# Performance work log

Hardware: AMD Instinct MI355X
Metric: run time of the kernel (lower is better)

## Reference

```python
import jax, jax.numpy as jnp
import numpy as np

S, B, H2, M = 4096, 16, 1024, 4096  # seq_len, batch, 2*hidden_size, max_number_of_entries


def setup_inputs() -> dict:
    key = jax.random.key(0)
    ks = jax.random.split(key, 5)
    return {
        "encoder_outputs": jax.random.normal(ks[0], (S, B, H2), jnp.float32),
        "state": jax.random.normal(ks[1], (B, H2), jnp.float32),
        "previous_attention": jax.random.uniform(ks[2], (B, M), jnp.float32),
        "attn_w": jax.random.normal(ks[3], (H2, H2), jnp.float32) / np.sqrt(H2).astype(np.float32),
        "attn_b": jnp.zeros((H2,), jnp.float32),
        "time_w": jax.random.normal(ks[4], (M, M), jnp.float32) / np.sqrt(M).astype(np.float32),
        "time_b": jnp.zeros((M,), jnp.float32),
    }


def reference(encoder_outputs, state, previous_attention, attn_w, attn_b, time_w, time_b):
    # encoder_outputs: [S, B, 2H]; state: [B, 2H]; previous_attention: [B, M]
    seq_len = encoder_outputs.shape[0]
    # attend(): Linear on state, then per-timestep dot product with encoder output.
    # The original Python loop over S timesteps + torch.cat is one batched matvec:
    altered_state = state @ attn_w.T + attn_b                      # [B, 2H]
    weights = jnp.einsum('bd,sbd->bs', altered_state, encoder_outputs)  # [B, S]
    # time_attention branch (its result is computed but unused by the outputs,
    # mirrored here for faithfulness to the original forward)
    apw = previous_attention @ time_w.T + time_b                   # [B, M]
    prev_probs = jax.nn.softmax(apw[:, :seq_len], axis=0)          # softmax over batch dim, as in original
    _adjusted_weights = prev_probs * weights                       # dead value in the original module
    # final softmax attention + weighted sum over encoder outputs
    normalized_weights = jax.nn.softmax(weights, axis=1)           # [B, S]
    attention_applied = jnp.einsum('bs,sbd->bd', normalized_weights, encoder_outputs)  # [B, 2H]
    return attention_applied, normalized_weights
```

## Files before the change

kernel.cpp:

```cpp
#include <hip/hip_runtime.h>
#include <cstdint>
#include <cstddef>

#define S_LEN 4096
#define B_SZ 16
#define H2D 1024
#define P_PER_B 256

__device__ __forceinline__ float dot4(float4 a, float4 b) {
    return a.x * b.x + a.y * b.y + a.z * b.z + a.w * b.w;
}
__device__ __forceinline__ void axpy4(float4& acc, float w, float4 v) {
    acc.x += w * v.x; acc.y += w * v.y; acc.z += w * v.z; acc.w += w * v.w;
}

__global__ __launch_bounds__(256) void k_altered(const float* __restrict__ state,
                                                 const float* __restrict__ attn_w,
                                                 const float* __restrict__ attn_b,
                                                 float* __restrict__ altered) {
    const int i = (blockIdx.x * 256 + threadIdx.x) >> 6;
    const int lane = threadIdx.x & 63;
    const float4* w4 = (const float4*)(attn_w + (size_t)i * H2D);
    float4 r[4];
#pragma unroll
    for (int j = 0; j < 4; ++j) r[j] = w4[lane + 64 * j];
    const float bias = attn_b[i];
    for (int b = 0; b < B_SZ; ++b) {
        const float4* s4 = (const float4*)(state + b * H2D);
        float p = 0.f;
#pragma unroll
        for (int j = 0; j < 4; ++j) p += dot4(r[j], s4[lane + 64 * j]);
#pragma unroll
        for (int off = 32; off; off >>= 1) p += __shfl_xor(p, off, 64);
        if (lane == 0) altered[b * H2D + i] = p + bias;
    }
}

__global__ __launch_bounds__(256) void k_pass1(const float* __restrict__ enc,
                                               const float* __restrict__ altered,
                                               float* __restrict__ w_raw) {
    const int b = blockIdx.y;
    const int wave = threadIdx.x >> 6, lane = threadIdx.x & 63;
    const int slot = blockIdx.x * 4 + wave;
    const float4* a4p = (const float4*)(altered + b * H2D);
    float4 af[4];
#pragma unroll
    for (int j = 0; j < 4; ++j) af[j] = a4p[lane + 64 * j];
    const int s0 = slot * 16;
    for (int k = 0; k < 16; k += 4) {
        float4 e[4][4];
#pragma unroll
        for (int r = 0; r < 4; ++r) {
            const float4* e4 = (const float4*)(enc + ((size_t)(s0 + k + r) * B_SZ + b) * H2D);
#pragma unroll
            for (int j = 0; j < 4; ++j) e[r][j] = e4[lane + 64 * j];
        }
        float p[4];
#pragma unroll
        for (int r = 0; r < 4; ++r) {
            p[r] = 0.f;
#pragma unroll
            for (int j = 0; j < 4; ++j) p[r] += dot4(af[j], e[r][j]);
        }
#pragma unroll
        for (int off = 32; off; off >>= 1) {
#pragma unroll
            for (int r = 0; r < 4; ++r) p[r] += __shfl_xor(p[r], off, 64);
        }
        if (lane == 0) {
#pragma unroll
            for (int r = 0; r < 4; ++r) w_raw[b * S_LEN + s0 + k + r] = p[r];
        }
    }
}

__global__ __launch_bounds__(1024) void k_softmax(const float* __restrict__ w_raw,
                                                  float* __restrict__ out_nw) {
    const int b = blockIdx.x, t = threadIdx.x;
    const int wave = t >> 6, lane = t & 63;
    __shared__ float sm[16], ss[16], sbc[2];
    float4 v = ((const float4*)(w_raw + b * S_LEN))[t];
    float m = fmaxf(fmaxf(v.x, v.y), fmaxf(v.z, v.w));
#pragma unroll
    for (int off = 32; off; off >>= 1) m = fmaxf(m, __shfl_xor(m, off, 64));
    if (lane == 0) sm[wave] = m;
    __syncthreads();
    if (t == 0) {
        float M = sm[0];
#pragma unroll
        for (int i = 1; i < 16; ++i) M = fmaxf(M, sm[i]);
        sbc[0] = M;
    }
    __syncthreads();
    const float M = sbc[0];
    float4 e;
    e.x = __expf(v.x - M); e.y = __expf(v.y - M);
    e.z = __expf(v.z - M); e.w = __expf(v.w - M);
    float s = e.x + e.y + e.z + e.w;
#pragma unroll
    for (int off = 32; off; off >>= 1) s += __shfl_xor(s, off, 64);
    if (lane == 0) ss[wave] = s;
    __syncthreads();
    if (t == 0) {
        float Z = 0.f;
#pragma unroll
        for (int i = 0; i < 16; ++i) Z += ss[i];
        sbc[1] = 1.f / Z;
    }
    __syncthreads();
    const float iZ = sbc[1];
    ((float4*)(out_nw + b * S_LEN))[t] = make_float4(e.x * iZ, e.y * iZ, e.z * iZ, e.w * iZ);
}

__global__ __launch_bounds__(256) void k_pass2(const float* __restrict__ enc,
                                               const float* __restrict__ nw,
                                               float* __restrict__ pacc) {
    const int b = blockIdx.y;
    const int wave = threadIdx.x >> 6, lane = threadIdx.x & 63;
    const int slot = blockIdx.x * 4 + wave;
    float4 acc[4];
#pragma unroll
    for (int j = 0; j < 4; ++j) acc[j] = make_float4(0.f, 0.f, 0.f, 0.f);
    const int s0 = slot * 16;
    for (int k = 0; k < 16; k += 4) {
        float4 e[4][4];
        float w[4];
#pragma unroll
        for (int r = 0; r < 4; ++r) {
            const int s = s0 + k + r;
            const float4* e4 = (const float4*)(enc + ((size_t)s * B_SZ + b) * H2D);
#pragma unroll
            for (int j = 0; j < 4; ++j) e[r][j] = e4[lane + 64 * j];
            w[r] = nw[b * S_LEN + s];
        }
#pragma unroll
        for (int r = 0; r < 4; ++r)
#pragma unroll
            for (int j = 0; j < 4; ++j) axpy4(acc[j], w[r], e[r][j]);
    }
    float4* o = (float4*)(pacc + (size_t)(b * P_PER_B + slot) * H2D);
#pragma unroll
    for (int j = 0; j < 4; ++j) o[lane + 64 * j] = acc[j];
}

__global__ __launch_bounds__(256) void k_comb1(const float* __restrict__ pacc,
                                               float* __restrict__ pacc2) {
    const int b = blockIdx.x >> 4, pg = blockIdx.x & 15, t = threadIdx.x;
    float4 s = make_float4(0.f, 0.f, 0.f, 0.f);
#pragma unroll
    for (int i = 0; i < 16; ++i) {
        const float4 v = ((const float4*)(pacc + (size_t)(b * P_PER_B + pg * 16 + i) * H2D))[t];
        s.x += v.x; s.y += v.y; s.z += v.z; s.w += v.w;
    }
    ((float4*)(pacc2 + (size_t)(b * 16 + pg) * H2D))[t] = s;
}

__global__ __launch_bounds__(64) void k_comb2(const float* __restrict__ pacc2,
                                              float* __restrict__ out_attn) {
    const int b = blockIdx.x >> 2;
    const int col = (blockIdx.x & 3) * 64 + threadIdx.x;
    float4 s = make_float4(0.f, 0.f, 0.f, 0.f);
#pragma unroll
    for (int i = 0; i < 16; ++i) {
        const float4 v = ((const float4*)(pacc2 + (size_t)(b * 16 + i) * H2D))[col];
        s.x += v.x; s.y += v.y; s.z += v.z; s.w += v.w;
    }
    ((float4*)(out_attn + b * H2D))[col] = s;
}

extern "C" void kernel_launch(void* const* d_in, const int* in_sizes, int n_in,
                              void* d_out, int out_size, void* d_ws, size_t ws_size,
                              hipStream_t stream) {
    const float* enc    = (const float*)d_in[0];
    const float* state  = (const float*)d_in[1];
    const float* attn_w = (const float*)d_in[3];
    const float* attn_b = (const float*)d_in[4];

    float* ws = (float*)d_ws;
    float* altered = ws;
    float* w_raw   = ws + 16384;
    float* pacc    = ws + 16384 + 65536;
    float* pacc2   = pacc + (size_t)B_SZ * P_PER_B * H2D;

    float* out_attn = (float*)d_out;
    float* out_nw   = (float*)d_out + B_SZ * H2D;

    hipLaunchKernelGGL(k_altered, dim3(256), dim3(256), 0, stream,
                       state, attn_w, attn_b, altered);
    hipLaunchKernelGGL(k_pass1, dim3(64, B_SZ), dim3(256), 0, stream,
                       enc, altered, w_raw);
    hipLaunchKernelGGL(k_softmax, dim3(B_SZ), dim3(1024), 0, stream,
                       w_raw, out_nw);
    hipLaunchKernelGGL(k_pass2, dim3(64, B_SZ), dim3(256), 0, stream,
                       enc, out_nw, pacc);
    hipLaunchKernelGGL(k_comb1, dim3(256), dim3(256), 0, stream,
                       pacc, pacc2);
    hipLaunchKernelGGL(k_comb2, dim3(64), dim3(64), 0, stream,
                       pacc2, out_attn);
}
```

Before: 450.0 us.

## Fuse score and weighted-sum passes with online softmax split-K combine

Merges the score pass and the weighted-sum pass into one flash-style kernel that keeps per-wave running max, sum and accumulator, so encoder outputs are streamed from memory once instead of twice. Finalization now rescales the per-slot partials by their exp-max correction, normalizes the weights, and reduces the partial accumulators with atomic adds. The exchange is extra exp/rescale arithmetic per chunk and a floating-point summation order that varies from run to run because of the atomics.

New measurement: 415.8 us. 7.6% less time.

```diff
diff --git a/kernel.cpp b/kernel.cpp
--- a/kernel.cpp
+++ b/kernel.cpp
@@ -36,26 +36,36 @@
     }
 }
 
-__global__ __launch_bounds__(256) void k_pass1(const float* __restrict__ enc,
+__global__ __launch_bounds__(256) void k_flash(const float* __restrict__ enc,
                                                const float* __restrict__ altered,
-                                               float* __restrict__ w_raw) {
+                                               float* __restrict__ w_raw,
+                                               float* __restrict__ pm,
+                                               float* __restrict__ pl,
+                                               float* __restrict__ pacc) {
     const int b = blockIdx.y;
     const int wave = threadIdx.x >> 6, lane = threadIdx.x & 63;
     const int slot = blockIdx.x * 4 + wave;
-    const float4* a4p = (const float4*)(altered + b * H2D);
+
+    const float4* a4 = (const float4*)(altered + b * H2D);
     float4 af[4];
 #pragma unroll
-    for (int j = 0; j < 4; ++j) af[j] = a4p[lane + 64 * j];
+    for (int j = 0; j < 4; ++j) af[j] = a4[lane + 64 * j];
+
+    float m = -1e30f, l = 0.f;
+    float4 acc[4];
+#pragma unroll
+    for (int j = 0; j < 4; ++j) acc[j] = make_float4(0.f, 0.f, 0.f, 0.f);
+
     const int s0 = slot * 16;
     for (int k = 0; k < 16; k += 4) {
         float4 e[4][4];
+        float p[4];
 #pragma unroll
         for (int r = 0; r < 4; ++r) {
             const float4* e4 = (const float4*)(enc + ((size_t)(s0 + k + r) * B_SZ + b) * H2D);
 #pragma unroll
             for (int j = 0; j < 4; ++j) e[r][j] = e4[lane + 64 * j];
         }
-        float p[4];
 #pragma unroll
         for (int r = 0; r < 4; ++r) {
             p[r] = 0.f;
@@ -63,109 +73,95 @@
             for (int j = 0; j < 4; ++j) p[r] += dot4(af[j], e[r][j]);
         }
 #pragma unroll
-        for (int off = 32; off; off >>= 1) {
+        for (int off = 32; off; off >>= 1)
 #pragma unroll
             for (int r = 0; r < 4; ++r) p[r] += __shfl_xor(p[r], off, 64);
-        }
         if (lane == 0) {
 #pragma unroll
             for (int r = 0; r < 4; ++r) w_raw[b * S_LEN + s0 + k + r] = p[r];
         }
+        float mn = m;
+#pragma unroll
+        for (int r = 0; r < 4; ++r) mn = fmaxf(mn, p[r]);
+        const float sc = __expf(m - mn);
+        float ex[4];
+#pragma unroll
+        for (int r = 0; r < 4; ++r) ex[r] = __expf(p[r] - mn);
+        l = l * sc + ex[0] + ex[1] + ex[2] + ex[3];
+#pragma unroll
+        for (int j = 0; j < 4; ++j) {
+            acc[j].x *= sc; acc[j].y *= sc; acc[j].z *= sc; acc[j].w *= sc;
+#pragma unroll
+            for (int r = 0; r < 4; ++r) axpy4(acc[j], ex[r], e[r][j]);
+        }
+        m = mn;
     }
-}
 
-__global__ __launch_bounds__(1024) void k_softmax(const float* __restrict__ w_raw,
-                                                  float* __restrict__ out_nw) {
-    const int b = blockIdx.x, t = threadIdx.x;
-    const int wave = t >> 6, lane = t & 63;
-    __shared__ float sm[16], ss[16], sbc[2];
-    float4 v = ((const float4*)(w_raw + b * S_LEN))[t];
-    float m = fmaxf(fmaxf(v.x, v.y), fmaxf(v.z, v.w));
-#pragma unroll
-    for (int off = 32; off; off >>= 1) m = fmaxf(m, __shfl_xor(m, off, 64));
-    if (lane == 0) sm[wave] = m;
-    __syncthreads();
-    if (t == 0) {
-        float M = sm[0];
-#pragma unroll
-        for (int i = 1; i < 16; ++i) M = fmaxf(M, sm[i]);
-        sbc[0] = M;
-    }
-    __syncthreads();
-    const float M = sbc[0];
-    float4 e;
-    e.x = __expf(v.x - M); e.y = __expf(v.y - M);
-    e.z = __expf(v.z - M); e.w = __expf(v.w - M);
-    float s = e.x + e.y + e.z + e.w;
-#pragma unroll
-    for (int off = 32; off; off >>= 1) s += __shfl_xor(s, off, 64);
-    if (lane == 0) ss[wave] = s;
-    __syncthreads();
-    if (t == 0) {
-        float Z = 0.f;
-#pragma unroll
-        for (int i = 0; i < 16; ++i) Z += ss[i];
-        sbc[1] = 1.f / Z;
-    }
-    __syncthreads();
-    const float iZ = sbc[1];
-    ((float4*)(out_nw + b * S_LEN))[t] = make_float4(e.x * iZ, e.y * iZ, e.z * iZ, e.w * iZ);
-}
-
-__global__ __launch_bounds__(256) void k_pass2(const float* __restrict__ enc,
-                                               const float* __restrict__ nw,
-                                               float* __restrict__ pacc) {
-    const int b = blockIdx.y;
-    const int wave = threadIdx.x >> 6, lane = threadIdx.x & 63;
-    const int slot = blockIdx.x * 4 + wave;
-    float4 acc[4];
-#pragma unroll
-    for (int j = 0; j < 4; ++j) acc[j] = make_float4(0.f, 0.f, 0.f, 0.f);
-    const int s0 = slot * 16;
-    for (int k = 0; k < 16; k += 4) {
-        float4 e[4][4];
-        float w[4];
-#pragma unroll
-        for (int r = 0; r < 4; ++r) {
-            const int s = s0 + k + r;
-            const float4* e4 = (const float4*)(enc + ((size_t)s * B_SZ + b) * H2D);
-#pragma unroll
-            for (int j = 0; j < 4; ++j) e[r][j] = e4[lane + 64 * j];
-            w[r] = nw[b * S_LEN + s];
-        }
-#pragma unroll
-        for (int r = 0; r < 4; ++r)
-#pragma unroll
-            for (int j = 0; j < 4; ++j) axpy4(acc[j], w[r], e[r][j]);
-    }
-    float4* o = (float4*)(pacc + (size_t)(b * P_PER_B + slot) * H2D);
+    const size_t pi = (size_t)(b * P_PER_B + slot);
+    if (lane == 0) { pm[pi] = m; pl[pi] = l; }
+    float4* o = (float4*)(pacc + pi * H2D);
 #pragma unroll
     for (int j = 0; j < 4; ++j) o[lane + 64 * j] = acc[j];
 }
 
-__global__ __launch_bounds__(256) void k_comb1(const float* __restrict__ pacc,
-                                               float* __restrict__ pacc2) {
-    const int b = blockIdx.x >> 4, pg = blockIdx.x & 15, t = threadIdx.x;
-    float4 s = make_float4(0.f, 0.f, 0.f, 0.f);
+__global__ __launch_bounds__(256) void k_fin1(const float* __restrict__ pm,
+                                              const float* __restrict__ pl,
+                                              const float* __restrict__ w_raw,
+                                              float* __restrict__ cexp,
+                                              float* __restrict__ MZ,
+                                              float* __restrict__ out_attn,
+                                              float* __restrict__ out_nw) {
+    const int b = blockIdx.x, t = threadIdx.x;
+    const int wave = t >> 6, lane = t & 63;
+    __shared__ float sw[4];
+    const float mv = pm[b * P_PER_B + t];
+    float mm = mv;
 #pragma unroll
-    for (int i = 0; i < 16; ++i) {
-        const float4 v = ((const float4*)(pacc + (size_t)(b * P_PER_B + pg * 16 + i) * H2D))[t];
-        s.x += v.x; s.y += v.y; s.z += v.z; s.w += v.w;
+    for (int off = 32; off; off >>= 1) mm = fmaxf(mm, __shfl_xor(mm, off, 64));
+    if (lane == 0) sw[wave] = mm;
+    __syncthreads();
+    const float M = fmaxf(fmaxf(sw[0], sw[1]), fmaxf(sw[2], sw[3]));
+    const float e = __expf(mv - M);
+    float zl = e * pl[b * P_PER_B + t];
+#pragma unroll
+    for (int off = 32; off; off >>= 1) zl += __shfl_xor(zl, off, 64);
+    __syncthreads();
+    if (lane == 0) sw[wave] = zl;
+    __syncthreads();
+    const float invZ = 1.f / (sw[0] + sw[1] + sw[2] + sw[3]);
+    cexp[b * P_PER_B + t] = e;
+    if (t == 0) { MZ[2 * b] = M; MZ[2 * b + 1] = invZ; }
+    ((float4*)(out_attn + b * H2D))[t] = make_float4(0.f, 0.f, 0.f, 0.f);
+    const float4* wr = (const float4*)(w_raw + b * S_LEN);
+    float4* on = (float4*)(out_nw + b * S_LEN);
+#pragma unroll
+    for (int i = 0; i < 4; ++i) {
+        const int idx = t + 256 * i;
+        const float4 v = wr[idx];
+        on[idx] = make_float4(__expf(v.x - M) * invZ, __expf(v.y - M) * invZ,
+                              __expf(v.z - M) * invZ, __expf(v.w - M) * invZ);
     }
-    ((float4*)(pacc2 + (size_t)(b * 16 + pg) * H2D))[t] = s;
 }
 
-__global__ __launch_bounds__(64) void k_comb2(const float* __restrict__ pacc2,
+__global__ __launch_bounds__(256) void k_fin2(const float* __restrict__ pacc,
+                                              const float* __restrict__ cexp,
+                                              const float* __restrict__ MZ,
                                               float* __restrict__ out_attn) {
-    const int b = blockIdx.x >> 2;
-    const int col = (blockIdx.x & 3) * 64 + threadIdx.x;
+    const int b = blockIdx.x, pg = blockIdx.y, t = threadIdx.x;
+    const float invZ = MZ[2 * b + 1];
+    const float* cb = cexp + b * P_PER_B + pg * 64;
+    const float4* base = (const float4*)(pacc + (size_t)(b * P_PER_B + pg * 64) * H2D);
     float4 s = make_float4(0.f, 0.f, 0.f, 0.f);
-#pragma unroll
-    for (int i = 0; i < 16; ++i) {
-        const float4 v = ((const float4*)(pacc2 + (size_t)(b * 16 + i) * H2D))[col];
-        s.x += v.x; s.y += v.y; s.z += v.z; s.w += v.w;
+#pragma unroll 8
+    for (int p = 0; p < 64; ++p) {
+        const float c = cb[p];
+        axpy4(s, c, base[(size_t)p * 256 + t]);
     }
-    ((float4*)(out_attn + b * H2D))[col] = s;
+    float* o = out_attn + b * H2D + 4 * t;
+    atomicAdd(o + 0, s.x * invZ);
+    atomicAdd(o + 1, s.y * invZ);
+    atomicAdd(o + 2, s.z * invZ);
+    atomicAdd(o + 3, s.w * invZ);
 }
 
 extern "C" void kernel_launch(void* const* d_in, const int* in_sizes, int n_in,
@@ -178,23 +174,22 @@
 
     float* ws = (float*)d_ws;
     float* altered = ws;
-    float* w_raw   = ws + 16384;
-    float* pacc    = ws + 16384 + 65536;
-    float* pacc2   = pacc + (size_t)B_SZ * P_PER_B * H2D;
+    float* w_raw   = altered + 16384;
+    float* pm      = w_raw + 65536;
+    float* pl      = pm + 4096;
+    float* cexp    = pl + 4096;
+    float* MZ      = cexp + 4096;
+    float* pacc    = MZ + 1024;
 
     float* out_attn = (float*)d_out;
     float* out_nw   = (float*)d_out + B_SZ * H2D;
 
     hipLaunchKernelGGL(k_altered, dim3(256), dim3(256), 0, stream,
                        state, attn_w, attn_b, altered);
-    hipLaunchKernelGGL(k_pass1, dim3(64, B_SZ), dim3(256), 0, stream,
-                       enc, altered, w_raw);
-    hipLaunchKernelGGL(k_softmax, dim3(B_SZ), dim3(1024), 0, stream,
-                       w_raw, out_nw);
-    hipLaunchKernelGGL(k_pass2, dim3(64, B_SZ), dim3(256), 0, stream,
-                       enc, out_nw, pacc);
-    hipLaunchKernelGGL(k_comb1, dim3(256), dim3(256), 0, stream,
-                       pacc, pacc2);
-    hipLaunchKernelGGL(k_comb2, dim3(64), dim3(64), 0, stream,
-                       pacc2, out_attn);
+    hipLaunchKernelGGL(k_flash, dim3(64, B_SZ), dim3(256), 0, stream,
+                       enc, altered, w_raw, pm, pl, pacc);
+    hipLaunchKernelGGL(k_fin1, dim3(B_SZ), dim3(256), 0, stream,
+                       pm, pl, w_raw, cexp, MZ, out_attn, out_nw);
+    hipLaunchKernelGGL(k_fin2, dim3(B_SZ, 4), dim3(256), 0, stream,
+                       pacc, cexp, MZ, out_attn);
 }
```
